# Kernel optimization log

Measured on AMD Instinct MI355X. Metric: run time of the kernel, lower is better.

Reference implementation:

```python
import jax, jax.numpy as jnp
import numpy as np

N = 100000
E = 1600000
F_IN = 128
HID = 64
C_OUT = 40


def gcn_conv(x, src, dst, W, b):
    # PyG GCNConv: linear transform, then symmetric-normalized sum aggregation
    n = x.shape[0]
    x = x @ W  # [N, out]
    deg = jax.ops.segment_sum(jnp.ones_like(src, dtype=x.dtype), dst, num_segments=n)
    dinv = jnp.where(deg > 0, jax.lax.rsqrt(deg), 0.0).astype(x.dtype)
    norm = dinv[src] * dinv[dst]  # [E']
    msgs = x[src] * norm[:, None]  # gather + scale
    out = jax.ops.segment_sum(msgs, dst, num_segments=n)  # scatter-add
    return out + b


def setup_inputs() -> dict:
    key = jax.random.key(0)
    k1, k2, k3, k4, k5, k6 = jax.random.split(key, 6)
    x = jax.random.normal(k1, (N, F_IN), dtype=jnp.float32)
    edge_index = jax.random.randint(k2, (2, E), 0, N, dtype=jnp.int64)
    # Glorot-style init for GCNConv linear weights, zero bias (PyG default)
    W1 = jax.random.normal(k3, (F_IN, HID), dtype=jnp.float32) / np.sqrt(F_IN)
    b1 = jnp.zeros((HID,), dtype=jnp.float32)
    W2 = jax.random.normal(k4, (HID, C_OUT), dtype=jnp.float32) / np.sqrt(HID)
    b2 = jnp.zeros((C_OUT,), dtype=jnp.float32)
    return {"x": x, "edge_index": edge_index, "W1": W1, "b1": b1, "W2": W2, "b2": b2}


def reference(x, edge_index, W1, b1, W2, b2):
    n = x.shape[0]
    # add self-loops (PyG GCNConv default add_self_loops=True)
    loops = jnp.arange(n, dtype=edge_index.dtype)
    src = jnp.concatenate([edge_index[0], loops])
    dst = jnp.concatenate([edge_index[1], loops])
    h = gcn_conv(x, src, dst, W1, b1)
    h = jax.nn.relu(h)
    # F.dropout with training=False is identity (eval-mode reference)
    out = gcn_conv(h, src, dst, W2, b2)
    return out
```

## Files before the change

### kernel.cpp

```cpp
#include <hip/hip_runtime.h>

#define F_IN 128
#define HID 64
#define C_OUT 40

#define RB_SHIFT 6
#define RB 64
#define CAP 1408
#define NBMAX 2048
#define FILL_CHUNK 8192
#define FILL_THREADS 512
#define AGG_BLOCKS 2048

#define MKBEG(node, b) (((node) >> RB_SHIFT) * CAP + (int)((b) >> 11))

typedef unsigned short ushort_t;
typedef unsigned int uint_t;
typedef __attribute__((ext_vector_type(8))) short bf16x8;
typedef __attribute__((ext_vector_type(4))) float f32x4;
typedef __attribute__((ext_vector_type(2))) float f32x2;

__device__ __forceinline__ ushort_t f2bf(float f) {
    uint_t u = __float_as_uint(f);
    return (ushort_t)((u + 0x7FFF + ((u >> 16) & 1)) >> 16);
}
__device__ __forceinline__ uint_t cvtpk(float lo, float hi) {
    uint_t r;
    asm("v_cvt_pk_bf16_f32 %0, %1, %2" : "=v"(r) : "v"(lo), "v"(hi));
    return r;
}
__device__ __forceinline__ float bf_lo(uint_t u) { return __uint_as_float(u << 16); }
__device__ __forceinline__ float bf_hi(uint_t u) { return __uint_as_float(u & 0xFFFF0000u); }
__device__ __forceinline__ bf16x8 u4_to_bf(uint4 u) {
    union { uint4 a; bf16x8 b; } cv; cv.a = u; return cv.b;
}

#define ACCP(u) { a[0] += (f32x2){bf_lo(u.x), bf_hi(u.x)}; \
                  a[1] += (f32x2){bf_lo(u.y), bf_hi(u.y)}; \
                  a[2] += (f32x2){bf_lo(u.z), bf_hi(u.z)}; \
                  a[3] += (f32x2){bf_lo(u.w), bf_hi(u.w)}; }

__global__ __launch_bounds__(FILL_THREADS) void bsort_kernel(
    const int* __restrict__ src, const int* __restrict__ dst, int E,
    int* __restrict__ hist, int* __restrict__ bm, int NB)
{
    __shared__ int lcnt[NBMAX];
    __shared__ int loff[NBMAX];
    __shared__ int wsum[8];
    int t = threadIdx.x;
    for (int i = t; i < NBMAX; i += FILL_THREADS) lcnt[i] = 0;
    __syncthreads();
    int base = blockIdx.x * FILL_CHUNK;
    int nE = min(E - base, FILL_CHUNK);
    #pragma unroll
    for (int k = 0; k < FILL_CHUNK / FILL_THREADS; ++k) {
        int e = k * FILL_THREADS + t;
        if (e < nE) atomicAdd(&lcnt[dst[base + e] >> RB_SHIFT], 1);
    }
    __syncthreads();
    {
        int v[4]; int tsum = 0;
        #pragma unroll
        for (int i = 0; i < 4; ++i) { v[i] = lcnt[t * 4 + i]; tsum += v[i]; }
        int lane = t & 63, wid = t >> 6;
        int incl = tsum;
        #pragma unroll
        for (int off = 1; off < 64; off <<= 1) {
            int u = __shfl_up(incl, off);
            if (lane >= off) incl += u;
        }
        if (lane == 63) wsum[wid] = incl;
        __syncthreads();
        if (t < 8) {
            int wv = wsum[t];
            int wincl = wv;
            #pragma unroll
            for (int off = 1; off < 8; off <<= 1) {
                int u = __shfl_up(wincl, off);
                if (t >= off) wincl += u;
            }
            wsum[t] = wincl - wv;
        }
        __syncthreads();
        int run = wsum[wid] + incl - tsum;
        #pragma unroll
        for (int i = 0; i < 4; ++i) { loff[t * 4 + i] = run; run += v[i]; }
    }
    __syncthreads();
    long long hrow = (long long)blockIdx.x * (NB + 1);
    for (int i = t; i < NB; i += FILL_THREADS) hist[hrow + i] = loff[i];
    if (t == 0) hist[hrow + NB] = nE;
    __syncthreads();
    #pragma unroll
    for (int k = 0; k < FILL_CHUNK / FILL_THREADS; ++k) {
        int e = k * FILL_THREADS + t;
        if (e < nE) {
            int d = dst[base + e], s = src[base + e];
            int b = d >> RB_SHIFT;
            int pos = atomicAdd(&loff[b], 1);
            bm[base + pos] = (s << RB_SHIFT) | (d & (RB - 1));
        }
    }
}

__global__ __launch_bounds__(256) void csr_gather_kernel(
    const int* __restrict__ hist, const int* __restrict__ bm, int K,
    int* __restrict__ csr, uint_t* __restrict__ bd,
    float* __restrict__ dinv, int N, int NB)
{
    __shared__ int staging[CAP];
    __shared__ int histo[RB];
    __shared__ int cursor[RB];
    __shared__ int waux[8];
    int t = threadIdx.x;
    int b = blockIdx.x;
    int len = 0, st = 0;
    if (t < K) {
        long long hrow = (long long)t * (NB + 1);
        st = hist[hrow + b];
        len = hist[hrow + b + 1] - st;
    }
    int lane = t & 63, wid = t >> 6;
    int incl = len;
    #pragma unroll
    for (int off = 1; off < 64; off <<= 1) {
        int u = __shfl_up(incl, off);
        if (lane >= off) incl += u;
    }
    if (lane == 63) waux[wid] = incl;
    if (t < RB) histo[t] = 0;
    __syncthreads();
    if (t < 4) {
        int w = waux[t];
        int wincl = w;
        #pragma unroll
        for (int off = 1; off < 4; off <<= 1) {
            int u = __shfl_up(wincl, off);
            if (t >= off) wincl += u;
        }
        waux[t] = wincl - w;
        if (t == 3) waux[4] = wincl;
    }
    __syncthreads();
    int bpos = waux[wid] + incl - len;
    int cnt = waux[4];
    if (cnt > CAP) cnt = CAP;
    if (t < K && len > 0) {
        int gbase = t * FILL_CHUNK + st;
        for (int i = 0; i < len; ++i) {
            int p = bpos + i;
            if (p < CAP) staging[p] = bm[gbase + i];
        }
    }
    __syncthreads();
    for (int i = t; i < cnt; i += 256) atomicAdd(&histo[staging[i] & (RB - 1)], 1);
    __syncthreads();
    if (t < RB) {
        int v = histo[t];
        int nincl = v;
        #pragma unroll
        for (int off = 1; off < 64; off <<= 1) {
            int u = __shfl_up(nincl, off);
            if (t >= off) nincl += u;
        }
        int excl = nincl - v;
        cursor[t] = excl;
        int node = b * RB + t;
        if (node < N) {
            bd[node] = ((uint_t)excl << 11) | (uint_t)v;
            dinv[node] = rsqrtf((float)(v + 1));
        }
    }
    __syncthreads();
    int cbase = b * CAP;
    for (int i = t; i < cnt; i += 256) {
        int e = staging[i];
        int n = e & (RB - 1);
        int r = atomicAdd(&cursor[n], 1);
        csr[cbase + r] = e >> RB_SHIFT;
    }
}

__global__ void wconv_kernel(const float* __restrict__ W1, const float* __restrict__ W2,
                             ushort_t* __restrict__ wb1, ushort_t* __restrict__ wb2)
{
    int tid = blockIdx.x * 256 + threadIdx.x;
    if (tid < 8192) {
        int j = tid & 7, l = (tid >> 3) & 63, ks = (tid >> 9) & 3, ct = tid >> 11;
        int c = ct * 16 + (l & 15);
        int k = ks * 32 + (l >> 4) * 8 + j;
        wb1[tid] = f2bf(W1[k * HID + c]);
    } else if (tid < 8192 + 3072) {
        int s = tid - 8192;
        int j = s & 7, l = (s >> 3) & 63, ks = (s >> 9) & 1, ct = s >> 10;
        int c = ct * 16 + (l & 15);
        int k = ks * 32 + (l >> 4) * 8 + j;
        wb2[s] = (c < C_OUT) ? f2bf(W2[k * C_OUT + c]) : (ushort_t)0;
    }
}

__global__ __launch_bounds__(256) void gemm1_mfma(
    const float* __restrict__ x, const uint_t* __restrict__ Wb,
    const float* __restrict__ dinv, uint_t* __restrict__ y, int N)
{
    __shared__ uint_t ldsW[4096];
    int t = threadIdx.x;
    {
        const uint4* s4 = (const uint4*)Wb;
        uint4* d4 = (uint4*)ldsW;
        for (int i = t; i < 1024; i += 256) d4[i] = s4[i];
    }
    __syncthreads();
    int wid = t >> 6, lane = t & 63;
    int m = lane & 15, kb = lane >> 4;
    int wr = blockIdx.x * 128 + wid * 32;
    int ra0 = min(wr + m, N - 1);
    int ra1 = min(wr + 16 + m, N - 1);
    f32x4 acc[2][4] = {};
    #pragma unroll
    for (int ks = 0; ks < 4; ++ks) {
        const float* p0 = &x[(size_t)ra0 * F_IN + ks * 32 + kb * 8];
        const float* p1 = &x[(size_t)ra1 * F_IN + ks * 32 + kb * 8];
        float4 a0 = *(const float4*)p0, a1 = *(const float4*)(p0 + 4);
        float4 c0 = *(const float4*)p1, c1 = *(const float4*)(p1 + 4);
        uint4 ua = make_uint4(cvtpk(a0.x, a0.y), cvtpk(a0.z, a0.w),
                              cvtpk(a1.x, a1.y), cvtpk(a1.z, a1.w));
        uint4 ub = make_uint4(cvtpk(c0.x, c0.y), cvtpk(c0.z, c0.w),
                              cvtpk(c1.x, c1.y), cvtpk(c1.z, c1.w));
        bf16x8 fa0 = u4_to_bf(ua), fa1 = u4_to_bf(ub);
        #pragma unroll
        for (int ct = 0; ct < 4; ++ct) {
            uint4 wu = *(uint4*)&ldsW[((ct * 4 + ks) * 64 + lane) * 4];
            bf16x8 fb = u4_to_bf(wu);
            acc[0][ct] = __builtin_amdgcn_mfma_f32_16x16x32_bf16(fa0, fb, acc[0][ct], 0, 0, 0);
            acc[1][ct] = __builtin_amdgcn_mfma_f32_16x16x32_bf16(fa1, fb, acc[1][ct], 0, 0, 0);
        }
    }
    int rq = lane >> 4;
    #pragma unroll
    for (int rt = 0; rt < 2; ++rt) {
        float dv[4]; int rows[4];
        #pragma unroll
        for (int j = 0; j < 4; ++j) {
            int r = wr + rt * 16 + rq * 4 + j;
            rows[j] = r;
            dv[j] = dinv[min(r, N - 1)];
        }
        #pragma unroll
        for (int ct = 0; ct < 4; ++ct) {
            #pragma unroll
            for (int j = 0; j < 4; ++j) {
                float v = acc[rt][ct][j] * dv[j];
                float pv = __shfl_xor(v, 1);
                if (!(lane & 1) && rows[j] < N) {
                    y[(size_t)rows[j] * 32 + ct * 8 + (m >> 1)] = cvtpk(v, pv);
                }
            }
        }
    }
}

__global__ __launch_bounds__(256) void agg1_kernel(
    const int* __restrict__ csr, const uint_t* __restrict__ bd,
    const uint_t* __restrict__ y, const float* __restrict__ dinv,
    const float* __restrict__ bias, uint_t* __restrict__ h, int N, int stride)
{
    int w = blockIdx.x * 4 + (threadIdx.x >> 6);
    if (w >= N) return;
    int lane = threadIdx.x & 63;
    int o = lane >> 3, c = lane & 7;
    int so = 2 * o;

    int n1 = w + stride, n2 = w + 2 * stride;
    uint_t bd0 = bd[w];
    uint_t bd1 = (n1 < N) ? bd[n1] : 0u;
    uint2 idx0;
    {
        int beg0 = MKBEG(w, bd0); int d0 = (int)(bd0 & 2047u);
        idx0.x = (so < d0) ? (uint_t)csr[beg0 + so] : 0xFFFFFFFFu;
        idx0.y = (so + 1 < d0) ? (uint_t)csr[beg0 + so + 1] : 0xFFFFFFFFu;
    }

    for (int node = w; node < N; ) {
        uint_t bd2 = (n2 < N) ? bd[n2] : 0u;
        uint2 idx1;
        {
            int beg1 = MKBEG(n1, bd1); int d1 = (int)(bd1 & 2047u);
            idx1.x = (so < d1) ? (uint_t)csr[beg1 + so] : 0xFFFFFFFFu;
            idx1.y = (so + 1 < d1) ? (uint_t)csr[beg1 + so + 1] : 0xFFFFFFFFu;
        }
        int deg0 = (int)(bd0 & 2047u);
        int beg0 = MKBEG(node, bd0);
        f32x2 a[4] = {};
        if (o == 0) {
            uint4 u = *(const uint4*)&y[(size_t)node * 32 + c * 4];
            ACCP(u);
        }
        uint2 cur = idx0;
        int j = 16;
        for (;;) {
            uint2 nxt = make_uint2(0xFFFFFFFFu, 0xFFFFFFFFu);
            bool more = (j < deg0);
            if (more) {
                int s = j + so;
                nxt.x = (s < deg0) ? (uint_t)csr[beg0 + s] : 0xFFFFFFFFu;
                nxt.y = (s + 1 < deg0) ? (uint_t)csr[beg0 + s + 1] : 0xFFFFFFFFu;
            }
            if (cur.x != 0xFFFFFFFFu) { uint4 u = *(const uint4*)&y[(size_t)cur.x * 32 + c * 4]; ACCP(u); }
            if (cur.y != 0xFFFFFFFFu) { uint4 u = *(const uint4*)&y[(size_t)cur.y * 32 + c * 4]; ACCP(u); }
            if (!more) break;
            cur = nxt; j += 16;
        }
        #pragma unroll
        for (int k = 0; k < 4; ++k) {
            a[k].x += __shfl_xor(a[k].x, 8);  a[k].y += __shfl_xor(a[k].y, 8);
            a[k].x += __shfl_xor(a[k].x, 16); a[k].y += __shfl_xor(a[k].y, 16);
            a[k].x += __shfl_xor(a[k].x, 32); a[k].y += __shfl_xor(a[k].y, 32);
        }
        if (o == 0) {
            float di = dinv[node];
            float4 b0 = *(const float4*)&bias[c * 8];
            float4 b1 = *(const float4*)&bias[c * 8 + 4];
            float o0 = fmaxf(a[0].x * di + b0.x, 0.f);
            float o1 = fmaxf(a[0].y * di + b0.y, 0.f);
            float o2 = fmaxf(a[1].x * di + b0.z, 0.f);
            float o3 = fmaxf(a[1].y * di + b0.w, 0.f);
            float o4 = fmaxf(a[2].x * di + b1.x, 0.f);
            float o5 = fmaxf(a[2].y * di + b1.y, 0.f);
            float o6 = fmaxf(a[3].x * di + b1.z, 0.f);
            float o7 = fmaxf(a[3].y * di + b1.w, 0.f);
            uint4 r = make_uint4(cvtpk(o0, o1), cvtpk(o2, o3), cvtpk(o4, o5), cvtpk(o6, o7));
            *(uint4*)&h[(size_t)node * 32 + c * 4] = r;
        }
        node = n1; n1 = n2; n2 += stride;
        bd0 = bd1; bd1 = bd2; idx0 = idx1;
    }
}

__global__ __launch_bounds__(256) void gemm2_mfma(
    const uint_t* __restrict__ h, const uint_t* __restrict__ Wb,
    const float* __restrict__ dinv, uint_t* __restrict__ y, int N)
{
    __shared__ uint_t ldsW[1536];
    int t = threadIdx.x;
    {
        const uint4* s4 = (const uint4*)Wb;
        uint4* d4 = (uint4*)ldsW;
        for (int i = t; i < 384; i += 256) d4[i] = s4[i];
    }
    __syncthreads();
    int wid = t >> 6, lane = t & 63;
    int m = lane & 15, kb = lane >> 4;
    int wr = blockIdx.x * 128 + wid * 32;
    int ra0 = min(wr + m, N - 1);
    int ra1 = min(wr + 16 + m, N - 1);
    f32x4 acc[2][3] = {};
    #pragma unroll
    for (int ks = 0; ks < 2; ++ks) {
        uint4 ua = *(const uint4*)&h[(size_t)ra0 * 32 + ks * 16 + kb * 4];
        uint4 ub = *(const uint4*)&h[(size_t)ra1 * 32 + ks * 16 + kb * 4];
        bf16x8 fa0 = u4_to_bf(ua), fa1 = u4_to_bf(ub);
        #pragma unroll
        for (int ct = 0; ct < 3; ++ct) {
            uint4 wu = *(uint4*)&ldsW[((ct * 2 + ks) * 64 + lane) * 4];
            bf16x8 fb = u4_to_bf(wu);
            acc[0][ct] = __builtin_amdgcn_mfma_f32_16x16x32_bf16(fa0, fb, acc[0][ct], 0, 0, 0);
            acc[1][ct] = __builtin_amdgcn_mfma_f32_16x16x32_bf16(fa1, fb, acc[1][ct], 0, 0, 0);
        }
    }
    int rq = lane >> 4;
    #pragma unroll
    for (int rt = 0; rt < 2; ++rt) {
        float dv[4]; int rows[4];
        #pragma unroll
        for (int j = 0; j < 4; ++j) {
            int r = wr + rt * 16 + rq * 4 + j;
            rows[j] = r;
            dv[j] = dinv[min(r, N - 1)];
        }
        #pragma unroll
        for (int ct = 0; ct < 3; ++ct) {
            #pragma unroll
            for (int j = 0; j < 4; ++j) {
                float v = acc[rt][ct][j] * dv[j];
                float pv = __shfl_xor(v, 1);
                bool colok = (ct < 2) || (m < 8);
                if (!(lane & 1) && colok && rows[j] < N) {
                    y[(size_t)rows[j] * 32 + ct * 8 + (m >> 1)] = cvtpk(v, pv);
                }
            }
        }
    }
}

__global__ __launch_bounds__(256) void agg2_kernel(
    const int* __restrict__ csr, const uint_t* __restrict__ bd,
    const uint_t* __restrict__ y, const float* __restrict__ dinv,
    const float* __restrict__ bias, float* __restrict__ out, int N, int stride)
{
    int w = blockIdx.x * 4 + (threadIdx.x >> 6);
    if (w >= N) return;
    int lane = threadIdx.x & 63;
    int o = lane >> 3, c = lane & 7;
    int so = 2 * o;
    bool act = (c < 5);

    int n1 = w + stride, n2 = w + 2 * stride;
    uint_t bd0 = bd[w];
    uint_t bd1 = (n1 < N) ? bd[n1] : 0u;
    uint2 idx0;
    {
        int beg0 = MKBEG(w, bd0); int d0 = (int)(bd0 & 2047u);
        idx0.x = (so < d0) ? (uint_t)csr[beg0 + so] : 0xFFFFFFFFu;
        idx0.y = (so + 1 < d0) ? (uint_t)csr[beg0 + so + 1] : 0xFFFFFFFFu;
    }

    for (int node = w; node < N; ) {
        uint_t bd2 = (n2 < N) ? bd[n2] : 0u;
        uint2 idx1;
        {
            int beg1 = MKBEG(n1, bd1); int d1 = (int)(bd1 & 2047u);
            idx1.x = (so < d1) ? (uint_t)csr[beg1 + so] : 0xFFFFFFFFu;
            idx1.y = (so + 1 < d1) ? (uint_t)csr[beg1 + so + 1] : 0xFFFFFFFFu;
        }
        int deg0 = (int)(bd0 & 2047u);
        int beg0 = MKBEG(node, bd0);
        f32x2 a[4] = {};
        if (o == 0 && act) {
            uint4 u = *(const uint4*)&y[(size_t)node * 32 + c * 4];
            ACCP(u);
        }
        uint2 cur = idx0;
        int j = 16;
        for (;;) {
            uint2 nxt = make_uint2(0xFFFFFFFFu, 0xFFFFFFFFu);
            bool more = (j < deg0);
            if (more) {
                int s = j + so;
                nxt.x = (s < deg0) ? (uint_t)csr[beg0 + s] : 0xFFFFFFFFu;
                nxt.y = (s + 1 < deg0) ? (uint_t)csr[beg0 + s + 1] : 0xFFFFFFFFu;
            }
            if (act && cur.x != 0xFFFFFFFFu) { uint4 u = *(const uint4*)&y[(size_t)cur.x * 32 + c * 4]; ACCP(u); }
            if (act && cur.y != 0xFFFFFFFFu) { uint4 u = *(const uint4*)&y[(size_t)cur.y * 32 + c * 4]; ACCP(u); }
            if (!more) break;
            cur = nxt; j += 16;
        }
        #pragma unroll
        for (int k = 0; k < 4; ++k) {
            a[k].x += __shfl_xor(a[k].x, 8);  a[k].y += __shfl_xor(a[k].y, 8);
            a[k].x += __shfl_xor(a[k].x, 16); a[k].y += __shfl_xor(a[k].y, 16);
            a[k].x += __shfl_xor(a[k].x, 32); a[k].y += __shfl_xor(a[k].y, 32);
        }
        if (o == 0 && act) {
            float di = dinv[node];
            float4 b0 = *(const float4*)&bias[c * 8];
            float4 b1 = *(const float4*)&bias[c * 8 + 4];
            float4 r0, r1;
            r0.x = a[0].x * di + b0.x;
            r0.y = a[0].y * di + b0.y;
            r0.z = a[1].x * di + b0.z;
            r0.w = a[1].y * di + b0.w;
            r1.x = a[2].x * di + b1.x;
            r1.y = a[2].y * di + b1.y;
            r1.z = a[3].x * di + b1.z;
            r1.w = a[3].y * di + b1.w;
            *(float4*)&out[(size_t)node * C_OUT + c * 8] = r0;
            *(float4*)&out[(size_t)node * C_OUT + c * 8 + 4] = r1;
        }
        node = n1; n1 = n2; n2 += stride;
        bd0 = bd1; bd1 = bd2; idx0 = idx1;
    }
}

extern "C" void kernel_launch(void* const* d_in, const int* in_sizes, int n_in,
                              void* d_out, int out_size, void* d_ws, size_t ws_size,
                              hipStream_t stream)
{
    const float* x  = (const float*)d_in[0];
    const int*   ei = (const int*)d_in[1];
    const float* W1 = (const float*)d_in[2];
    const float* b1 = (const float*)d_in[3];
    const float* W2 = (const float*)d_in[4];
    const float* b2 = (const float*)d_in[5];
    float* out = (float*)d_out;

    int N = in_sizes[0] / F_IN;
    int E = in_sizes[1] / 2;
    const int* src = ei;
    const int* dst = ei + E;
    int NB = (N + RB - 1) / RB;
    int K = (E + FILL_CHUNK - 1) / FILL_CHUNK;
    int NBLK = (N + 127) / 128;
    int aggStride = AGG_BLOCKS * 4;

    char* ws = (char*)d_ws;
    uint_t* y1b    = (uint_t*)ws;  ws += (size_t)N * 32 * 4;
    uint_t* y2b    = (uint_t*)ws;  ws += (size_t)N * 32 * 4;
    uint_t* h1p    = (uint_t*)ws;  ws += (size_t)N * 32 * 4;
    float* dinv    = (float*)ws;   ws += (size_t)N * 4;
    uint_t* bd     = (uint_t*)ws;  ws += (size_t)N * 4;
    int*   hist    = (int*)ws;     ws += (size_t)K * (NB + 1) * 4;
    int*   bm      = (int*)ws;     ws += (size_t)K * FILL_CHUNK * 4;
    int*   csr     = (int*)ws;     ws += (size_t)NB * CAP * 4;
    ushort_t* wb1  = (ushort_t*)ws; ws += 8192 * 2;
    ushort_t* wb2  = (ushort_t*)ws; ws += 3072 * 2;

    wconv_kernel<<<44, 256, 0, stream>>>(W1, W2, wb1, wb2);

    bsort_kernel<<<K, FILL_THREADS, 0, stream>>>(src, dst, E, hist, bm, NB);
    csr_gather_kernel<<<NB, 256, 0, stream>>>(hist, bm, K, csr, bd, dinv, N, NB);

    gemm1_mfma<<<NBLK, 256, 0, stream>>>(x, (const uint_t*)wb1, dinv, y1b, N);
    agg1_kernel<<<AGG_BLOCKS, 256, 0, stream>>>(csr, bd, y1b, dinv, b1, h1p, N, aggStride);

    gemm2_mfma<<<NBLK, 256, 0, stream>>>(h1p, (const uint_t*)wb2, dinv, y2b, N);
    agg2_kernel<<<AGG_BLOCKS, 256, 0, stream>>>(csr, bd, y2b, dinv, b2, out, N, aggStride);
}
```

Measured before the change: 148.4 us.

## Pad per-node CSR rows to 16-edge windows with a zero sentinel row

Each node's neighbour list in the bucketed CSR is padded to a multiple of 16 entries, and the padding is filled with index N, which points at an extra all-zero row appended to y1b and y2b. The aggregation kernels then load neighbour indices as aligned uint2 pairs and run a fixed number of windows with no per-edge bounds or sentinel checks. This removes branches and divergence from the gather loops. In exchange the CSR capacity grows, an extra pass pre-fills the CSR, and the padded entries cost wasted gathers of the zero row.

```diff
diff --git a/kernel.cpp b/kernel.cpp
--- a/kernel.cpp
+++ b/kernel.cpp
@@ -6,13 +6,14 @@
 
 #define RB_SHIFT 6
 #define RB 64
-#define CAP 1408
+#define CAP 2176
 #define NBMAX 2048
 #define FILL_CHUNK 8192
 #define FILL_THREADS 512
 #define AGG_BLOCKS 2048
 
-#define MKBEG(node, b) (((node) >> RB_SHIFT) * CAP + (int)((b) >> 11))
+#define MKBEG(node, b) (((node) >> RB_SHIFT) * CAP + (((int)((b) >> 8)) << 4))
+#define NWIN(b) ((int)((b) & 255u))
 
 typedef unsigned short ushort_t;
 typedef unsigned int uint_t;
@@ -157,34 +158,45 @@
     __syncthreads();
     if (t < RB) {
         int v = histo[t];
-        int nincl = v;
+        int vv = v ? v : 1;
+        int pv = (vv + 15) & ~15;
+        int nincl = pv;
         #pragma unroll
         for (int off = 1; off < 64; off <<= 1) {
             int u = __shfl_up(nincl, off);
             if (t >= off) nincl += u;
         }
-        int excl = nincl - v;
+        int excl = nincl - pv;
         cursor[t] = excl;
+        if (t == 63) waux[5] = (nincl <= CAP) ? nincl : CAP;
         int node = b * RB + t;
         if (node < N) {
-            bd[node] = ((uint_t)excl << 11) | (uint_t)v;
+            bd[node] = ((uint_t)(excl >> 4) << 8) | (uint_t)(pv >> 4);
             dinv[node] = rsqrtf((float)(v + 1));
         }
     }
     __syncthreads();
     int cbase = b * CAP;
+    int totp = waux[5];
+    for (int i = t; i < totp; i += 256) csr[cbase + i] = N;
+    __syncthreads();
     for (int i = t; i < cnt; i += 256) {
         int e = staging[i];
         int n = e & (RB - 1);
         int r = atomicAdd(&cursor[n], 1);
-        csr[cbase + r] = e >> RB_SHIFT;
+        if (r < CAP) csr[cbase + r] = e >> RB_SHIFT;
     }
 }
 
 __global__ void wconv_kernel(const float* __restrict__ W1, const float* __restrict__ W2,
-                             ushort_t* __restrict__ wb1, ushort_t* __restrict__ wb2)
+                             ushort_t* __restrict__ wb1, ushort_t* __restrict__ wb2,
+                             uint_t* __restrict__ y1b, uint_t* __restrict__ y2b, int N)
 {
     int tid = blockIdx.x * 256 + threadIdx.x;
+    if (blockIdx.x == 0 && threadIdx.x < 32) {
+        y1b[(size_t)N * 32 + threadIdx.x] = 0u;
+        y2b[(size_t)N * 32 + threadIdx.x] = 0u;
+    }
     if (tid < 8192) {
         int j = tid & 7, l = (tid >> 3) & 63, ks = (tid >> 9) & 3, ct = tid >> 11;
         int c = ct * 16 + (l & 15);
@@ -274,22 +286,13 @@
     int n1 = w + stride, n2 = w + 2 * stride;
     uint_t bd0 = bd[w];
     uint_t bd1 = (n1 < N) ? bd[n1] : 0u;
-    uint2 idx0;
-    {
-        int beg0 = MKBEG(w, bd0); int d0 = (int)(bd0 & 2047u);
-        idx0.x = (so < d0) ? (uint_t)csr[beg0 + so] : 0xFFFFFFFFu;
-        idx0.y = (so + 1 < d0) ? (uint_t)csr[beg0 + so + 1] : 0xFFFFFFFFu;
-    }
+    uint2 idx0 = *(const uint2*)&csr[MKBEG(w, bd0) + so];
 
     for (int node = w; node < N; ) {
         uint_t bd2 = (n2 < N) ? bd[n2] : 0u;
-        uint2 idx1;
-        {
-            int beg1 = MKBEG(n1, bd1); int d1 = (int)(bd1 & 2047u);
-            idx1.x = (so < d1) ? (uint_t)csr[beg1 + so] : 0xFFFFFFFFu;
-            idx1.y = (so + 1 < d1) ? (uint_t)csr[beg1 + so + 1] : 0xFFFFFFFFu;
-        }
-        int deg0 = (int)(bd0 & 2047u);
+        uint2 idx1 = make_uint2((uint_t)N, (uint_t)N);
+        if (n1 < N) idx1 = *(const uint2*)&csr[MKBEG(n1, bd1) + so];
+        int nw = NWIN(bd0);
         int beg0 = MKBEG(node, bd0);
         f32x2 a[4] = {};
         if (o == 0) {
@@ -297,19 +300,15 @@
             ACCP(u);
         }
         uint2 cur = idx0;
-        int j = 16;
-        for (;;) {
-            uint2 nxt = make_uint2(0xFFFFFFFFu, 0xFFFFFFFFu);
-            bool more = (j < deg0);
-            if (more) {
-                int s = j + so;
-                nxt.x = (s < deg0) ? (uint_t)csr[beg0 + s] : 0xFFFFFFFFu;
-                nxt.y = (s + 1 < deg0) ? (uint_t)csr[beg0 + s + 1] : 0xFFFFFFFFu;
-            }
-            if (cur.x != 0xFFFFFFFFu) { uint4 u = *(const uint4*)&y[(size_t)cur.x * 32 + c * 4]; ACCP(u); }
-            if (cur.y != 0xFFFFFFFFu) { uint4 u = *(const uint4*)&y[(size_t)cur.y * 32 + c * 4]; ACCP(u); }
-            if (!more) break;
-            cur = nxt; j += 16;
+        for (int wd = 1; wd < nw; ++wd) {
+            uint2 nxt = *(const uint2*)&csr[beg0 + wd * 16 + so];
+            uint4 u0 = *(const uint4*)&y[(size_t)cur.x * 32 + c * 4]; ACCP(u0);
+            uint4 u1 = *(const uint4*)&y[(size_t)cur.y * 32 + c * 4]; ACCP(u1);
+            cur = nxt;
+        }
+        {
+            uint4 u0 = *(const uint4*)&y[(size_t)cur.x * 32 + c * 4]; ACCP(u0);
+            uint4 u1 = *(const uint4*)&y[(size_t)cur.y * 32 + c * 4]; ACCP(u1);
         }
         #pragma unroll
         for (int k = 0; k < 4; ++k) {
@@ -408,22 +407,13 @@
     int n1 = w + stride, n2 = w + 2 * stride;
     uint_t bd0 = bd[w];
     uint_t bd1 = (n1 < N) ? bd[n1] : 0u;
-    uint2 idx0;
-    {
-        int beg0 = MKBEG(w, bd0); int d0 = (int)(bd0 & 2047u);
-        idx0.x = (so < d0) ? (uint_t)csr[beg0 + so] : 0xFFFFFFFFu;
-        idx0.y = (so + 1 < d0) ? (uint_t)csr[beg0 + so + 1] : 0xFFFFFFFFu;
-    }
+    uint2 idx0 = *(const uint2*)&csr[MKBEG(w, bd0) + so];
 
     for (int node = w; node < N; ) {
         uint_t bd2 = (n2 < N) ? bd[n2] : 0u;
-        uint2 idx1;
-        {
-            int beg1 = MKBEG(n1, bd1); int d1 = (int)(bd1 & 2047u);
-            idx1.x = (so < d1) ? (uint_t)csr[beg1 + so] : 0xFFFFFFFFu;
-            idx1.y = (so + 1 < d1) ? (uint_t)csr[beg1 + so + 1] : 0xFFFFFFFFu;
-        }
-        int deg0 = (int)(bd0 & 2047u);
+        uint2 idx1 = make_uint2((uint_t)N, (uint_t)N);
+        if (n1 < N) idx1 = *(const uint2*)&csr[MKBEG(n1, bd1) + so];
+        int nw = NWIN(bd0);
         int beg0 = MKBEG(node, bd0);
         f32x2 a[4] = {};
         if (o == 0 && act) {
@@ -431,19 +421,17 @@
             ACCP(u);
         }
         uint2 cur = idx0;
-        int j = 16;
-        for (;;) {
-            uint2 nxt = make_uint2(0xFFFFFFFFu, 0xFFFFFFFFu);
-            bool more = (j < deg0);
-            if (more) {
-                int s = j + so;
-                nxt.x = (s < deg0) ? (uint_t)csr[beg0 + s] : 0xFFFFFFFFu;
-                nxt.y = (s + 1 < deg0) ? (uint_t)csr[beg0 + s + 1] : 0xFFFFFFFFu;
+        for (int wd = 1; wd < nw; ++wd) {
+            uint2 nxt = *(const uint2*)&csr[beg0 + wd * 16 + so];
+            if (act) {
+                uint4 u0 = *(const uint4*)&y[(size_t)cur.x * 32 + c * 4]; ACCP(u0);
+                uint4 u1 = *(const uint4*)&y[(size_t)cur.y * 32 + c * 4]; ACCP(u1);
             }
-            if (act && cur.x != 0xFFFFFFFFu) { uint4 u = *(const uint4*)&y[(size_t)cur.x * 32 + c * 4]; ACCP(u); }
-            if (act && cur.y != 0xFFFFFFFFu) { uint4 u = *(const uint4*)&y[(size_t)cur.y * 32 + c * 4]; ACCP(u); }
-            if (!more) break;
-            cur = nxt; j += 16;
+            cur = nxt;
+        }
+        if (act) {
+            uint4 u0 = *(const uint4*)&y[(size_t)cur.x * 32 + c * 4]; ACCP(u0);
+            uint4 u1 = *(const uint4*)&y[(size_t)cur.y * 32 + c * 4]; ACCP(u1);
         }
         #pragma unroll
         for (int k = 0; k < 4; ++k) {
@@ -494,8 +482,8 @@
     int aggStride = AGG_BLOCKS * 4;
 
     char* ws = (char*)d_ws;
-    uint_t* y1b    = (uint_t*)ws;  ws += (size_t)N * 32 * 4;
-    uint_t* y2b    = (uint_t*)ws;  ws += (size_t)N * 32 * 4;
+    uint_t* y1b    = (uint_t*)ws;  ws += (size_t)(N + 1) * 32 * 4;
+    uint_t* y2b    = (uint_t*)ws;  ws += (size_t)(N + 1) * 32 * 4;
     uint_t* h1p    = (uint_t*)ws;  ws += (size_t)N * 32 * 4;
     float* dinv    = (float*)ws;   ws += (size_t)N * 4;
     uint_t* bd     = (uint_t*)ws;  ws += (size_t)N * 4;
@@ -505,7 +493,7 @@
     ushort_t* wb1  = (ushort_t*)ws; ws += 8192 * 2;
     ushort_t* wb2  = (ushort_t*)ws; ws += 3072 * 2;
 
-    wconv_kernel<<<44, 256, 0, stream>>>(W1, W2, wb1, wb2);
+    wconv_kernel<<<44, 256, 0, stream>>>(W1, W2, wb1, wb2, y1b, y2b, N);
 
     bsort_kernel<<<K, FILL_THREADS, 0, stream>>>(src, dst, E, hist, bm, NB);
     csr_gather_kernel<<<NB, 256, 0, stream>>>(hist, bm, K, csr, bd, dinv, N, NB);
```

New measurement: 141.5 us (median of 2 runs). -4.6%, faster.
